# Performance work log

Hardware: AMD Instinct MI355X
Metric: run time of the kernel (lower is better)

Reference implementation:

```python
import jax, jax.numpy as jnp
import numpy as np

N_NODES = 100000
N_EDGES = 1600000
IN_DIM = 128
HEADS = 4
HEAD_DIM = 16  # hidden_dim 64 // 4 heads
HID = HEADS * HEAD_DIM
NEG_SLOPE = 0.2


def setup_inputs() -> dict:
    key = jax.random.key(0)
    ks = jax.random.split(key, 20)
    inp = {
        "x": jax.random.normal(ks[0], (N_NODES, IN_DIM), dtype=jnp.float32),
        "edge_index": jax.random.randint(ks[1], (2, N_EDGES), 0, N_NODES, dtype=jnp.int32),
    }
    dims = [IN_DIM, HID, HID]
    for l in range(3):
        d_in = dims[l]
        sc = 1.0 / np.sqrt(d_in)
        inp[f"w{l}"] = jax.random.normal(ks[2 + 4 * l], (d_in, HID), dtype=jnp.float32) * sc
        inp[f"asrc{l}"] = jax.random.normal(ks[3 + 4 * l], (HEADS, HEAD_DIM), dtype=jnp.float32) * 0.1
        inp[f"adst{l}"] = jax.random.normal(ks[4 + 4 * l], (HEADS, HEAD_DIM), dtype=jnp.float32) * 0.1
        inp[f"b{l}"] = jnp.zeros((HID,), dtype=jnp.float32)
    inp["out_w"] = jax.random.normal(ks[14], (HID, 1), dtype=jnp.float32) * (1.0 / np.sqrt(HID))
    inp["out_b"] = jnp.zeros((1,), dtype=jnp.float32)
    return inp


def _gat_layer(h, src, dst, W, a_src, a_dst, b):
    # h: [N, d_in]; src/dst: [E'] (self-loops already appended)
    n = h.shape[0]
    xh = (h @ W).reshape(n, HEADS, HEAD_DIM)              # [N,H,C]
    al_s = jnp.sum(xh * a_src, axis=-1)                   # [N,H]
    al_d = jnp.sum(xh * a_dst, axis=-1)                   # [N,H]
    e = jax.nn.leaky_relu(al_s[src] + al_d[dst], NEG_SLOPE)  # [E',H]
    # segment-softmax over incoming edges of each destination node
    m = jax.ops.segment_max(e, dst, num_segments=n)       # [N,H]
    p = jnp.exp(e - m[dst])
    z = jax.ops.segment_sum(p, dst, num_segments=n)       # [N,H]
    alpha = p / (z[dst] + 1e-16)                          # [E',H]
    msg = xh[src] * alpha[:, :, None]                     # [E',H,C]
    out = jax.ops.segment_sum(msg, dst, num_segments=n)   # [N,H,C]
    return out.reshape(n, HID) + b


def reference(x, edge_index, w0, asrc0, adst0, b0, w1, asrc1, adst1, b1,
              w2, asrc2, adst2, b2, out_w, out_b):
    n = x.shape[0]
    loops = jnp.arange(n, dtype=edge_index.dtype)
    src = jnp.concatenate([edge_index[0], loops])  # PyG GATConv adds self-loops
    dst = jnp.concatenate([edge_index[1], loops])
    h = x
    params = [(w0, asrc0, adst0, b0), (w1, asrc1, adst1, b1), (w2, asrc2, adst2, b2)]
    for W, a_s, a_d, b in params:
        h = _gat_layer(h, src, dst, W, a_s, a_d, b)
        h = jax.nn.relu(h)
    return (h @ out_w + out_b).squeeze(-1)  # [N]
```

## Files before the change

### kernel.cpp

```cpp
#include <hip/hip_runtime.h>


#define NBMAX 512
#define SCHUNK 4096
#define BCAP 8192
#define PADSLACK 768

typedef __attribute__((ext_vector_type(8))) short bf16x8;
typedef __attribute__((ext_vector_type(4))) float f32x4;

__device__ inline unsigned short bf16_rtn(float x) {
    union { float f; unsigned u; } a; a.f = x;
    return (unsigned short)((a.u + 0x7FFFu + ((a.u >> 16) & 1u)) >> 16);
}
__device__ inline float bf16_to_f(unsigned short s) {
    union { unsigned u; float f; } b; b.u = ((unsigned)s) << 16;
    return b.f;
}

__global__ __launch_bounds__(256) void k_init(int* __restrict__ bhist, int nb,
                                              float* __restrict__ als, float* __restrict__ xh, int n) {
    int i = blockIdx.x * 256 + threadIdx.x;
    if (i < nb) bhist[i] = 0;
    int j = i - NBMAX;
    if (j >= 0 && j < 4) als[(size_t)n * 4 + j] = -1e30f;
    int k = i - NBMAX - 4;
    if (k >= 0 && k < 64) xh[(size_t)n * 64 + k] = 0.f;
}

__global__ __launch_bounds__(256) void k_bhist(const int* __restrict__ dst, int* __restrict__ bhist, int e) {
    __shared__ unsigned int h[NBMAX];
    int t = threadIdx.x;
    h[t] = 0;
    h[t + 256] = 0;
    __syncthreads();
    for (int i = blockIdx.x * 256 + t; i < e; i += gridDim.x * 256)
        atomicAdd(&h[dst[i] >> 8], 1u);
    __syncthreads();
    if (h[t]) atomicAdd(&bhist[t], (int)h[t]);
    if (h[t + 256]) atomicAdd(&bhist[t + 256], (int)h[t + 256]);
}

__global__ __launch_bounds__(512) void k_bscan(const int* __restrict__ bhist, int* __restrict__ boffs,
                                               int* __restrict__ bfill, int nb, int e) {
    __shared__ int s[NBMAX];
    int t = threadIdx.x;
    int v = (t < nb) ? bhist[t] : 0;
    s[t] = v;
    __syncthreads();
    for (int o = 1; o < 512; o <<= 1) {
        int add = (t >= o) ? s[t - o] : 0;
        __syncthreads();
        s[t] += add;
        __syncthreads();
    }
    boffs[t] = s[t] - v;
    if (t == 511) boffs[512] = s[511];
    bfill[t] = 0;
}

__global__ __launch_bounds__(512) void k_bscatter(const int* __restrict__ src, const int* __restrict__ dst,
                                                  const int* __restrict__ boffs, int* __restrict__ bfill,
                                                  unsigned int* __restrict__ edata, int e) {
    __shared__ unsigned int hist[NBMAX];
    __shared__ unsigned int loc[NBMAX];
    __shared__ int gbase[NBMAX];
    __shared__ unsigned int stmp[NBMAX];
    __shared__ unsigned int sortbuf[SCHUNK];
    __shared__ int posbuf[SCHUNK];
    int t = threadIdx.x;
    int i0 = blockIdx.x * SCHUNK;
    int cnt = min(SCHUNK, e - i0);
    hist[t] = 0;
    __syncthreads();
    for (int j = t; j < cnt; j += 512) atomicAdd(&hist[dst[i0 + j] >> 8], 1u);
    __syncthreads();
    unsigned int v = hist[t];
    stmp[t] = v;
    __syncthreads();
    for (int o = 1; o < 512; o <<= 1) {
        unsigned int add = (t >= o) ? stmp[t - o] : 0;
        __syncthreads();
        stmp[t] += add;
        __syncthreads();
    }
    loc[t] = stmp[t] - v;
    int gb = 0;
    if (v > 0) gb = atomicAdd(&bfill[t], (int)v);
    gbase[t] = boffs[t] + gb - (int)loc[t];
    hist[t] = loc[t];
    __syncthreads();
    for (int j = t; j < cnt; j += 512) {
        int d = dst[i0 + j];
        int s = src[i0 + j];
        int b = d >> 8;
        unsigned int p = atomicAdd(&hist[b], 1u);
        sortbuf[p] = (unsigned int)s | ((unsigned int)(d & 255) << 24);
        posbuf[p] = gbase[b] + (int)p;
    }
    __syncthreads();
    for (int j = t; j < cnt; j += 512) edata[posbuf[j]] = sortbuf[j];
}

__global__ __launch_bounds__(256) void k_bfinal(const unsigned int* __restrict__ edata,
                                                const int* __restrict__ boffs, int* __restrict__ poffs,
                                                int* __restrict__ pend, int* __restrict__ ssrc,
                                                int n, int nb) {
    __shared__ unsigned int hist[256];
    __shared__ unsigned int stmp[256];
    __shared__ unsigned int loc[256];
    __shared__ unsigned int cnt_s[256];
    __shared__ unsigned int srcbuf[BCAP];
    int b = blockIdx.x;
    int t = threadIdx.x;
    int e0 = boffs[b], e1 = boffs[b + 1];
    int cnt = e1 - e0;
    int pb = e0 + b * PADSLACK;
    hist[t] = 0;
    __syncthreads();
    for (int j = t; j < cnt; j += 256) atomicAdd(&hist[edata[e0 + j] >> 24], 1u);
    __syncthreads();
    unsigned int v = hist[t];
    unsigned int v4 = (v + 3u) & ~3u;
    cnt_s[t] = v;
    stmp[t] = v4;
    __syncthreads();
    for (int o = 1; o < 256; o <<= 1) {
        unsigned int add = (t >= o) ? stmp[t - o] : 0;
        __syncthreads();
        stmp[t] += add;
        __syncthreads();
    }
    loc[t] = stmp[t] - v4;
    int ptot = (int)stmp[255];
    int node = b * 256 + t;
    if (node < n) {
        poffs[node] = pb + (int)loc[t];
        pend[node] = pb + (int)(loc[t] + v4);
    }
    hist[t] = loc[t];
    __syncthreads();
    if (cnt + PADSLACK <= BCAP) {
        for (int j = t; j < cnt; j += 256) {
            unsigned int p = edata[e0 + j];
            unsigned int pos = atomicAdd(&hist[p >> 24], 1u);
            srcbuf[pos] = p & 0xFFFFFFu;
        }
        for (unsigned int k = v; k < v4; ++k) srcbuf[loc[t] + k] = (unsigned int)n;
        __syncthreads();
        for (int j = t; j < ptot; j += 256) ssrc[pb + j] = (int)srcbuf[j];
    } else {
        for (int j = t; j < cnt; j += 256) {
            unsigned int p = edata[e0 + j];
            unsigned int pos = atomicAdd(&hist[p >> 24], 1u);
            ssrc[pb + (int)pos] = (int)(p & 0xFFFFFFu);
        }
        for (unsigned int k = v; k < v4; ++k) ssrc[pb + (int)(loc[t] + k)] = n;
    }
}

__global__ __launch_bounds__(256) void k_wprep(const float* __restrict__ w0, const float* __restrict__ w1,
                                               const float* __restrict__ w2,
                                               unsigned short* __restrict__ p0h, unsigned short* __restrict__ p0l,
                                               unsigned short* __restrict__ p1h, unsigned short* __restrict__ p1l,
                                               unsigned short* __restrict__ p2h, unsigned short* __restrict__ p2l) {
    int g = blockIdx.x * 256 + threadIdx.x;
    const float* W;
    unsigned short *ph, *pl;
    int idx;
    if (g < 1024) { W = w0; ph = p0h; pl = p0l; idx = g; }
    else if (g < 1536) { W = w1; ph = p1h; pl = p1l; idx = g - 1024; }
    else if (g < 2048) { W = w2; ph = p2h; pl = p2l; idx = g - 1536; }
    else return;
    int ko = idx >> 6, nn = idx & 63;
#pragma unroll
    for (int j = 0; j < 8; ++j) {
        float w = W[(size_t)(ko * 8 + j) * 64 + nn];
        unsigned short hb = bf16_rtn(w);
        ph[(size_t)idx * 8 + j] = hb;
        pl[(size_t)idx * 8 + j] = bf16_rtn(w - bf16_to_f(hb));
    }
}

template <int D_IN>
__global__ __launch_bounds__(256) void k_mgemm(const float* __restrict__ h,
                                               const unsigned short* __restrict__ wph,
                                               const unsigned short* __restrict__ wpl,
                                               const float* __restrict__ asrc, const float* __restrict__ adst,
                                               float* __restrict__ xh, float* __restrict__ als,
                                               float* __restrict__ ald, int n) {
    int t = threadIdx.x;
    int wv = t >> 6, lane = t & 63;
    int quad = lane >> 4, l16 = lane & 15;
    int m0 = blockIdx.x * 64 + wv * 16;
    int node_a = m0 + l16;
    int mm = min(node_a, n - 1);
    const float* hrow = h + (size_t)mm * D_IN + quad * 8;

    f32x4 acc[4];
#pragma unroll
    for (int i = 0; i < 4; ++i) acc[i] = (f32x4){0.f, 0.f, 0.f, 0.f};

    constexpr int KSTEPS = D_IN / 32;
#pragma unroll
    for (int s = 0; s < KSTEPS; ++s) {
        float4 a0 = *(const float4*)(hrow + s * 32);
        float4 a1 = *(const float4*)(hrow + s * 32 + 4);
        float av[8] = {a0.x, a0.y, a0.z, a0.w, a1.x, a1.y, a1.z, a1.w};
        bf16x8 ahi, alo;
#pragma unroll
        for (int j = 0; j < 8; ++j) {
            unsigned short hb = bf16_rtn(av[j]);
            ahi[j] = (short)hb;
            alo[j] = (short)bf16_rtn(av[j] - bf16_to_f(hb));
        }
        const unsigned short* bbase = wph + ((size_t)((s * 4 + quad) * 64 + l16)) * 8;
        const unsigned short* bbasel = wpl + ((size_t)((s * 4 + quad) * 64 + l16)) * 8;
#pragma unroll
        for (int nt = 0; nt < 4; ++nt) {
            bf16x8 bhi = *(const bf16x8*)(bbase + (size_t)nt * 16 * 8);
            bf16x8 blo = *(const bf16x8*)(bbasel + (size_t)nt * 16 * 8);
            acc[nt] = __builtin_amdgcn_mfma_f32_16x16x32_bf16(ahi, bhi, acc[nt], 0, 0, 0);
            acc[nt] = __builtin_amdgcn_mfma_f32_16x16x32_bf16(ahi, blo, acc[nt], 0, 0, 0);
            acc[nt] = __builtin_amdgcn_mfma_f32_16x16x32_bf16(alo, bhi, acc[nt], 0, 0, 0);
        }
    }
#pragma unroll
    for (int nt = 0; nt < 4; ++nt) {
        float as_l = asrc[nt * 16 + l16];
        float ad_l = adst[nt * 16 + l16];
#pragma unroll
        for (int r = 0; r < 4; ++r) {
            int node = m0 + quad * 4 + r;
            float c = acc[nt][r];
            if (node < n) xh[(size_t)node * 64 + nt * 16 + l16] = c;
            float ps = c * as_l, pd = c * ad_l;
            ps += __shfl_xor(ps, 1, 64); pd += __shfl_xor(pd, 1, 64);
            ps += __shfl_xor(ps, 2, 64); pd += __shfl_xor(pd, 2, 64);
            ps += __shfl_xor(ps, 4, 64); pd += __shfl_xor(pd, 4, 64);
            ps += __shfl_xor(ps, 8, 64); pd += __shfl_xor(pd, 8, 64);
            if (l16 == 0 && node < n) {
                als[node * 4 + nt] = ps;
                ald[node * 4 + nt] = pd;
            }
        }
    }
}

__device__ inline float4 lrelu4(float4 v) {
    float4 r;
    r.x = v.x >= 0.f ? v.x : 0.2f * v.x;
    r.y = v.y >= 0.f ? v.y : 0.2f * v.y;
    r.z = v.z >= 0.f ? v.z : 0.2f * v.z;
    r.w = v.w >= 0.f ? v.w : 0.2f * v.w;
    return r;
}

#define ACCUM(LO, HI, ACC, ZS)                                                  \
    {                                                                           \
        int g_ = ((LO) - s0) >> 2, gb_ = ((HI) - s0) >> 2;                      \
        for (; g_ + 4 <= gb_; g_ += 4) {                                        \
            int4 uu0 = *(const int4*)&ub[g_ * 4];                               \
            int4 uu1 = *(const int4*)&ub[g_ * 4 + 4];                           \
            int4 uu2 = *(const int4*)&ub[g_ * 4 + 8];                           \
            int4 uu3 = *(const int4*)&ub[g_ * 4 + 12];                          \
            float4 pp0 = *(const float4*)&per[g_ * 4];                          \
            float4 pp1 = *(const float4*)&per[g_ * 4 + 4];                      \
            float4 pp2 = *(const float4*)&per[g_ * 4 + 8];                      \
            float4 pp3 = *(const float4*)&per[g_ * 4 + 12];                     \
            float x0 = *(const float*)(xl + (size_t)(unsigned)uu0.x);           \
            float x1 = *(const float*)(xl + (size_t)(unsigned)uu0.y);           \
            float x2 = *(const float*)(xl + (size_t)(unsigned)uu0.z);           \
            float x3 = *(const float*)(xl + (size_t)(unsigned)uu0.w);           \
            float x4 = *(const float*)(xl + (size_t)(unsigned)uu1.x);           \
            float x5 = *(const float*)(xl + (size_t)(unsigned)uu1.y);           \
            float x6 = *(const float*)(xl + (size_t)(unsigned)uu1.z);           \
            float x7 = *(const float*)(xl + (size_t)(unsigned)uu1.w);           \
            float x8 = *(const float*)(xl + (size_t)(unsigned)uu2.x);           \
            float x9 = *(const float*)(xl + (size_t)(unsigned)uu2.y);           \
            float xa = *(const float*)(xl + (size_t)(unsigned)uu2.z);           \
            float xb = *(const float*)(xl + (size_t)(unsigned)uu2.w);           \
            float xc = *(const float*)(xl + (size_t)(unsigned)uu3.x);           \
            float xd = *(const float*)(xl + (size_t)(unsigned)uu3.y);           \
            float xe = *(const float*)(xl + (size_t)(unsigned)uu3.z);           \
            float xf = *(const float*)(xl + (size_t)(unsigned)uu3.w);           \
            ZS += pp0.x + pp0.y + pp0.z + pp0.w;                                \
            ZS += pp1.x + pp1.y + pp1.z + pp1.w;                                \
            ZS += pp2.x + pp2.y + pp2.z + pp2.w;                                \
            ZS += pp3.x + pp3.y + pp3.z + pp3.w;                                \
            ACC += pp0.x * x0; ACC += pp0.y * x1; ACC += pp0.z * x2; ACC += pp0.w * x3; \
            ACC += pp1.x * x4; ACC += pp1.y * x5; ACC += pp1.z * x6; ACC += pp1.w * x7; \
            ACC += pp2.x * x8; ACC += pp2.y * x9; ACC += pp2.z * xa; ACC += pp2.w * xb; \
            ACC += pp3.x * xc; ACC += pp3.y * xd; ACC += pp3.z * xe; ACC += pp3.w * xf; \
        }                                                                       \
        for (; g_ < gb_; ++g_) {                                                \
            int4 uu = *(const int4*)&ub[g_ * 4];                                \
            float4 pp = *(const float4*)&per[g_ * 4];                           \
            float x0 = *(const float*)(xl + (size_t)(unsigned)uu.x);            \
            float x1 = *(const float*)(xl + (size_t)(unsigned)uu.y);            \
            float x2 = *(const float*)(xl + (size_t)(unsigned)uu.z);            \
            float x3 = *(const float*)(xl + (size_t)(unsigned)uu.w);            \
            ZS += pp.x + pp.y + pp.z + pp.w;                                    \
            ACC += pp.x * x0; ACC += pp.y * x1; ACC += pp.z * x2; ACC += pp.w * x3; \
        }                                                                       \
    }

__global__ __launch_bounds__(256) void k_agg(const float* __restrict__ xh,
                                             const float* __restrict__ als, const float* __restrict__ ald,
                                             const int* __restrict__ poffs, const int* __restrict__ pend,
                                             const int* __restrict__ ssrc,
                                             const float* __restrict__ bias, float* __restrict__ hout,
                                             const float* __restrict__ outw, const float* __restrict__ outb,
                                             float* __restrict__ fout, int n) {
    __shared__ int s_u[4][64];
    __shared__ float s_pe[4][4][64];
    int wslot = threadIdx.x >> 6;
    int lane = threadIdx.x & 63;
    int w = (blockIdx.x * 256 + threadIdx.x) >> 6;
    int v0 = w << 2;
    if (v0 >= n) return;
    int head = lane >> 4;
    int* ub = s_u[wslot];
    float* per = s_pe[wslot][head];
    float* pew = &s_pe[wslot][0][lane];

    int vlast = n - 1;
    int last = min(v0 + 3, vlast);
    int4 rr = *(const int4*)(poffs + v0);
    int e3 = pend[last];
    int r0 = rr.x;
    int r1 = (v0 + 1 <= last) ? rr.y : e3;
    int r2 = (v0 + 2 <= last) ? rr.z : e3;
    int r3 = (v0 + 3 <= last) ? rr.w : e3;

    const char* xl = (const char*)(xh + lane);
    float acc0 = *(const float*)(xl + ((size_t)(unsigned)v0 << 8));
    float acc1 = *(const float*)(xl + ((size_t)(unsigned)min(v0 + 1, vlast) << 8));
    float acc2 = *(const float*)(xl + ((size_t)(unsigned)min(v0 + 2, vlast) << 8));
    float acc3 = *(const float*)(xl + ((size_t)(unsigned)min(v0 + 3, vlast) << 8));
    float zs0 = 0.f, zs1 = 0.f, zs2 = 0.f, zs3 = 0.f;

    for (int s0 = r0; s0 < e3; s0 += 64) {
        int cnt = min(64, e3 - s0);
        int e = s0 + lane;
        int u = n;
        if (lane < cnt) u = ssrc[e];
        int nid = v0 + (e >= r1) + (e >= r2) + (e >= r3);
        nid = min(nid, vlast);
        float4 alsd = *(const float4*)(als + 4 * (size_t)nid);
        float4 aldd = *(const float4*)(ald + 4 * (size_t)nid);
        float4 m4 = lrelu4(make_float4(alsd.x + aldd.x, alsd.y + aldd.y,
                                       alsd.z + aldd.z, alsd.w + aldd.w));
        float4 alu = *(const float4*)(als + 4 * (size_t)u);
        float4 e4 = lrelu4(make_float4(alu.x + aldd.x, alu.y + aldd.y,
                                       alu.z + aldd.z, alu.w + aldd.w));
        float4 pe;
        pe.x = __expf(e4.x - m4.x);
        pe.y = __expf(e4.y - m4.y);
        pe.z = __expf(e4.z - m4.z);
        pe.w = __expf(e4.w - m4.w);
        ub[lane] = u << 8;
        pew[0] = pe.x;
        pew[64] = pe.y;
        pew[128] = pe.z;
        pew[192] = pe.w;
        int lim = s0 + cnt;
        int hi0 = min(r1, lim);
        int lo1 = max(r1, s0), hi1 = min(r2, lim);
        int lo2 = max(r2, s0), hi2 = min(r3, lim);
        int lo3 = max(r3, s0);
        ACCUM(s0, hi0, acc0, zs0);
        ACCUM(lo1, hi1, acc1, zs1);
        ACCUM(lo2, hi2, acc2, zs2);
        ACCUM(lo3, lim, acc3, zs3);
    }

    float bl = bias[lane];
    float z0 = 1.f + zs0, z1 = 1.f + zs1, z2 = 1.f + zs2, z3 = 1.f + zs3;
    float o0 = fmaxf(acc0 / (z0 + 1e-16f) + bl, 0.f);
    float o1 = fmaxf(acc1 / (z1 + 1e-16f) + bl, 0.f);
    float o2 = fmaxf(acc2 / (z2 + 1e-16f) + bl, 0.f);
    float o3 = fmaxf(acc3 / (z3 + 1e-16f) + bl, 0.f);
    if (outw) {
        float ow = outw[lane];
        float ob = outb[0];
        float t0 = o0 * ow, t1 = o1 * ow, t2 = o2 * ow, t3 = o3 * ow;
#pragma unroll
        for (int d = 32; d; d >>= 1) {
            t0 += __shfl_down(t0, d, 64);
            t1 += __shfl_down(t1, d, 64);
            t2 += __shfl_down(t2, d, 64);
            t3 += __shfl_down(t3, d, 64);
        }
        if (lane == 0) {
            fout[v0] = t0 + ob;
            if (v0 + 1 < n) fout[v0 + 1] = t1 + ob;
            if (v0 + 2 < n) fout[v0 + 2] = t2 + ob;
            if (v0 + 3 < n) fout[v0 + 3] = t3 + ob;
        }
    } else {
        hout[((size_t)v0 << 6) + lane] = o0;
        if (v0 + 1 < n) hout[((size_t)(v0 + 1) << 6) + lane] = o1;
        if (v0 + 2 < n) hout[((size_t)(v0 + 2) << 6) + lane] = o2;
        if (v0 + 3 < n) hout[((size_t)(v0 + 3) << 6) + lane] = o3;
    }
}

extern "C" void kernel_launch(void* const* d_in, const int* in_sizes, int n_in,
                              void* d_out, int out_size, void* d_ws, size_t ws_size,
                              hipStream_t stream) {
    const float* x = (const float*)d_in[0];
    const int* ei = (const int*)d_in[1];
    const float* w[3] = {(const float*)d_in[2], (const float*)d_in[6], (const float*)d_in[10]};
    const float* as[3] = {(const float*)d_in[3], (const float*)d_in[7], (const float*)d_in[11]};
    const float* ad[3] = {(const float*)d_in[4], (const float*)d_in[8], (const float*)d_in[12]};
    const float* b[3] = {(const float*)d_in[5], (const float*)d_in[9], (const float*)d_in[13]};
    const float* outw = (const float*)d_in[14];
    const float* outb = (const float*)d_in[15];

    const int N = in_sizes[0] / 128;
    const int E = in_sizes[1] / 2;
    const int* src = ei;
    const int* dst = ei + E;
    const int NB = (N + 255) / 256;

    char* ws = (char*)d_ws;
    auto alloc = [&](size_t bytes) -> void* {
        void* p = (void*)ws;
        ws += (bytes + 255) & ~(size_t)255;
        return p;
    };
    int* bhist = (int*)alloc(NBMAX * 4);
    int* boffs = (int*)alloc((NBMAX + 1) * 4);
    int* bfill = (int*)alloc(NBMAX * 4);
    int* poffs = (int*)alloc((size_t)(N + 8) * 4);
    int* pend = (int*)alloc((size_t)N * 4);
    int* ssrc = (int*)alloc((size_t)(E + NBMAX * PADSLACK + 256) * 4);
    float* xh = (float*)alloc((size_t)(N + 1) * 64 * 4);
    float* hbuf = (float*)alloc((size_t)N * 64 * 4);
    float* als = (float*)alloc((size_t)(N + 1) * 4 * 4);
    float* ald = (float*)alloc((size_t)N * 4 * 4);
    unsigned short* p0h = (unsigned short*)alloc(8192 * 2);
    unsigned short* p0l = (unsigned short*)alloc(8192 * 2);
    unsigned short* p1h = (unsigned short*)alloc(4096 * 2);
    unsigned short* p1l = (unsigned short*)alloc(4096 * 2);
    unsigned short* p2h = (unsigned short*)alloc(4096 * 2);
    unsigned short* p2l = (unsigned short*)alloc(4096 * 2);
    unsigned int* edata = (unsigned int*)xh;

    k_wprep<<<8, 256, 0, stream>>>(w[0], w[1], w[2], p0h, p0l, p1h, p1l, p2h, p2l);
    k_init<<<3, 256, 0, stream>>>(bhist, NBMAX, als, xh, N);
    k_bhist<<<256, 256, 0, stream>>>(dst, bhist, E);
    k_bscan<<<1, 512, 0, stream>>>(bhist, boffs, bfill, NB, E);
    k_bscatter<<<(E + SCHUNK - 1) / SCHUNK, 512, 0, stream>>>(src, dst, boffs, bfill, edata, E);
    k_bfinal<<<NB, 256, 0, stream>>>(edata, boffs, poffs, pend, ssrc, N, NB);

    const int gblocks = (N + 63) / 64;
    const int ablocks = (N + 15) / 16;

    k_mgemm<128><<<gblocks, 256, 0, stream>>>(x, p0h, p0l, as[0], ad[0], xh, als, ald, N);
    k_agg<<<ablocks, 256, 0, stream>>>(xh, als, ald, poffs, pend, ssrc, b[0], hbuf, nullptr, nullptr, nullptr, N);
    k_mgemm<64><<<gblocks, 256, 0, stream>>>(hbuf, p1h, p1l, as[1], ad[1], xh, als, ald, N);
    k_agg<<<ablocks, 256, 0, stream>>>(xh, als, ald, poffs, pend, ssrc, b[1], hbuf, nullptr, nullptr, nullptr, N);
    k_mgemm<64><<<gblocks, 256, 0, stream>>>(hbuf, p2h, p2l, as[2], ad[2], xh, als, ald, N);
    k_agg<<<ablocks, 256, 0, stream>>>(xh, als, ald, poffs, pend, ssrc, b[2], nullptr, outw, outb, (float*)d_out, N);
}
```

Before: 434.3 us.

## Replace bucketed CSR build with degree-count scan scatter; prefetch and split accumulators in agg

```diff
diff --git a/kernel.cpp b/kernel.cpp
--- a/kernel.cpp
+++ b/kernel.cpp
@@ -1,10 +1,7 @@
 #include <hip/hip_runtime.h>
 
 
-#define NBMAX 512
-#define SCHUNK 4096
-#define BCAP 8192
-#define PADSLACK 768
+#define SCB 2048
 
 typedef __attribute__((ext_vector_type(8))) short bf16x8;
 typedef __attribute__((ext_vector_type(4))) float f32x4;
@@ -18,145 +15,97 @@
     return b.f;
 }
 
-__global__ __launch_bounds__(256) void k_init(int* __restrict__ bhist, int nb,
+__global__ __launch_bounds__(256) void k_init(int* __restrict__ deg,
                                               float* __restrict__ als, float* __restrict__ xh, int n) {
     int i = blockIdx.x * 256 + threadIdx.x;
-    if (i < nb) bhist[i] = 0;
-    int j = i - NBMAX;
-    if (j >= 0 && j < 4) als[(size_t)n * 4 + j] = -1e30f;
-    int k = i - NBMAX - 4;
-    if (k >= 0 && k < 64) xh[(size_t)n * 64 + k] = 0.f;
-}
-
-__global__ __launch_bounds__(256) void k_bhist(const int* __restrict__ dst, int* __restrict__ bhist, int e) {
-    __shared__ unsigned int h[NBMAX];
-    int t = threadIdx.x;
-    h[t] = 0;
-    h[t + 256] = 0;
-    __syncthreads();
-    for (int i = blockIdx.x * 256 + t; i < e; i += gridDim.x * 256)
-        atomicAdd(&h[dst[i] >> 8], 1u);
-    __syncthreads();
-    if (h[t]) atomicAdd(&bhist[t], (int)h[t]);
-    if (h[t + 256]) atomicAdd(&bhist[t + 256], (int)h[t + 256]);
-}
-
-__global__ __launch_bounds__(512) void k_bscan(const int* __restrict__ bhist, int* __restrict__ boffs,
-                                               int* __restrict__ bfill, int nb, int e) {
-    __shared__ int s[NBMAX];
-    int t = threadIdx.x;
-    int v = (t < nb) ? bhist[t] : 0;
-    s[t] = v;
-    __syncthreads();
-    for (int o = 1; o < 512; o <<= 1) {
-        int add = (t >= o) ? s[t - o] : 0;
-        __syncthreads();
-        s[t] += add;
-        __syncthreads();
-    }
-    boffs[t] = s[t] - v;
-    if (t == 511) boffs[512] = s[511];
-    bfill[t] = 0;
-}
-
-__global__ __launch_bounds__(512) void k_bscatter(const int* __restrict__ src, const int* __restrict__ dst,
-                                                  const int* __restrict__ boffs, int* __restrict__ bfill,
-                                                  unsigned int* __restrict__ edata, int e) {
-    __shared__ unsigned int hist[NBMAX];
-    __shared__ unsigned int loc[NBMAX];
-    __shared__ int gbase[NBMAX];
-    __shared__ unsigned int stmp[NBMAX];
-    __shared__ unsigned int sortbuf[SCHUNK];
-    __shared__ int posbuf[SCHUNK];
-    int t = threadIdx.x;
-    int i0 = blockIdx.x * SCHUNK;
-    int cnt = min(SCHUNK, e - i0);
-    hist[t] = 0;
-    __syncthreads();
-    for (int j = t; j < cnt; j += 512) atomicAdd(&hist[dst[i0 + j] >> 8], 1u);
-    __syncthreads();
-    unsigned int v = hist[t];
-    stmp[t] = v;
-    __syncthreads();
-    for (int o = 1; o < 512; o <<= 1) {
-        unsigned int add = (t >= o) ? stmp[t - o] : 0;
-        __syncthreads();
-        stmp[t] += add;
-        __syncthreads();
-    }
-    loc[t] = stmp[t] - v;
-    int gb = 0;
-    if (v > 0) gb = atomicAdd(&bfill[t], (int)v);
-    gbase[t] = boffs[t] + gb - (int)loc[t];
-    hist[t] = loc[t];
-    __syncthreads();
-    for (int j = t; j < cnt; j += 512) {
-        int d = dst[i0 + j];
-        int s = src[i0 + j];
-        int b = d >> 8;
-        unsigned int p = atomicAdd(&hist[b], 1u);
-        sortbuf[p] = (unsigned int)s | ((unsigned int)(d & 255) << 24);
-        posbuf[p] = gbase[b] + (int)p;
-    }
-    __syncthreads();
-    for (int j = t; j < cnt; j += 512) edata[posbuf[j]] = sortbuf[j];
-}
-
-__global__ __launch_bounds__(256) void k_bfinal(const unsigned int* __restrict__ edata,
-                                                const int* __restrict__ boffs, int* __restrict__ poffs,
-                                                int* __restrict__ pend, int* __restrict__ ssrc,
-                                                int n, int nb) {
-    __shared__ unsigned int hist[256];
-    __shared__ unsigned int stmp[256];
-    __shared__ unsigned int loc[256];
-    __shared__ unsigned int cnt_s[256];
-    __shared__ unsigned int srcbuf[BCAP];
-    int b = blockIdx.x;
-    int t = threadIdx.x;
-    int e0 = boffs[b], e1 = boffs[b + 1];
-    int cnt = e1 - e0;
-    int pb = e0 + b * PADSLACK;
-    hist[t] = 0;
-    __syncthreads();
-    for (int j = t; j < cnt; j += 256) atomicAdd(&hist[edata[e0 + j] >> 24], 1u);
-    __syncthreads();
-    unsigned int v = hist[t];
-    unsigned int v4 = (v + 3u) & ~3u;
-    cnt_s[t] = v;
-    stmp[t] = v4;
+    if (i < n) deg[i] = 0;
+    if (i < 4) als[(size_t)n * 4 + i] = -1e30f;
+    if (i < 64) xh[(size_t)n * 64 + i] = 0.f;
+}
+
+__global__ __launch_bounds__(256) void k_deg(const int* __restrict__ dst, int* __restrict__ deg, int e) {
+    int i = blockIdx.x * 256 + threadIdx.x;
+    if (i < e) atomicAdd(&deg[dst[i]], 1);
+}
+
+__global__ __launch_bounds__(256) void k_scan1(const int* __restrict__ deg, int* __restrict__ loc,
+                                               int* __restrict__ bsum, int n) {
+    __shared__ int ts[256];
+    int b = blockIdx.x, t = threadIdx.x;
+    int base = b * SCB + t * 8;
+    int d[8], s = 0;
+    if (base + 8 <= n) {
+        int4 a = *(const int4*)(deg + base);
+        int4 c = *(const int4*)(deg + base + 4);
+        int dv[8] = {a.x, a.y, a.z, a.w, c.x, c.y, c.z, c.w};
+#pragma unroll
+        for (int k = 0; k < 8; ++k) { d[k] = s; s += (dv[k] + 3) & ~3; }
+    } else {
+#pragma unroll
+        for (int k = 0; k < 8; ++k) {
+            d[k] = s;
+            int v = (base + k < n) ? deg[base + k] : 0;
+            s += (v + 3) & ~3;
+        }
+    }
+    ts[t] = s;
     __syncthreads();
     for (int o = 1; o < 256; o <<= 1) {
-        unsigned int add = (t >= o) ? stmp[t - o] : 0;
+        int add = (t >= o) ? ts[t - o] : 0;
         __syncthreads();
-        stmp[t] += add;
+        ts[t] += add;
         __syncthreads();
     }
-    loc[t] = stmp[t] - v4;
-    int ptot = (int)stmp[255];
-    int node = b * 256 + t;
-    if (node < n) {
-        poffs[node] = pb + (int)loc[t];
-        pend[node] = pb + (int)(loc[t] + v4);
-    }
-    hist[t] = loc[t];
-    __syncthreads();
-    if (cnt + PADSLACK <= BCAP) {
-        for (int j = t; j < cnt; j += 256) {
-            unsigned int p = edata[e0 + j];
-            unsigned int pos = atomicAdd(&hist[p >> 24], 1u);
-            srcbuf[pos] = p & 0xFFFFFFu;
-        }
-        for (unsigned int k = v; k < v4; ++k) srcbuf[loc[t] + k] = (unsigned int)n;
-        __syncthreads();
-        for (int j = t; j < ptot; j += 256) ssrc[pb + j] = (int)srcbuf[j];
+    int excl = ts[t] - s;
+    if (base + 8 <= n) {
+        int4 o0 = {excl + d[0], excl + d[1], excl + d[2], excl + d[3]};
+        int4 o1 = {excl + d[4], excl + d[5], excl + d[6], excl + d[7]};
+        *(int4*)(loc + base) = o0;
+        *(int4*)(loc + base + 4) = o1;
     } else {
-        for (int j = t; j < cnt; j += 256) {
-            unsigned int p = edata[e0 + j];
-            unsigned int pos = atomicAdd(&hist[p >> 24], 1u);
-            ssrc[pb + (int)pos] = (int)(p & 0xFFFFFFu);
-        }
-        for (unsigned int k = v; k < v4; ++k) ssrc[pb + (int)(loc[t] + k)] = n;
-    }
+        for (int k = 0; k < 8; ++k)
+            if (base + k < n) loc[base + k] = excl + d[k];
+    }
+    if (t == 255) bsum[b] = ts[255];
+}
+
+__global__ __launch_bounds__(64) void k_scan2(int* __restrict__ bsum, int nb) {
+    int t = threadIdx.x;
+    int v = (t < nb) ? bsum[t] : 0;
+#pragma unroll
+    for (int o = 1; o < 64; o <<= 1) {
+        int u = __shfl_up(v, o, 64);
+        if (t >= o) v += u;
+    }
+    if (t < nb) bsum[t] = v;
+}
+
+__global__ __launch_bounds__(256) void k_scan3(const int* __restrict__ deg, const int* __restrict__ loc,
+                                               const int* __restrict__ bsum, int* __restrict__ poffs,
+                                               int* __restrict__ pend, int* __restrict__ cursor, int n) {
+    int i = blockIdx.x * 256 + threadIdx.x;
+    if (i >= n) return;
+    int b = i >> 11;
+    int base = b ? bsum[b - 1] : 0;
+    int p = base + loc[i];
+    int d4 = (deg[i] + 3) & ~3;
+    poffs[i] = p;
+    pend[i] = p + d4;
+    cursor[i] = p;
+}
+
+__global__ __launch_bounds__(256) void k_fill(int4* __restrict__ ssrc4, int n, int tot4) {
+    int i = blockIdx.x * 256 + threadIdx.x;
+    if (i < tot4) ssrc4[i] = (int4){n, n, n, n};
+}
+
+__global__ __launch_bounds__(256) void k_scatter(const int* __restrict__ src, const int* __restrict__ dst,
+                                                 int* __restrict__ cursor, int* __restrict__ ssrc, int e) {
+    int i = blockIdx.x * 256 + threadIdx.x;
+    if (i >= e) return;
+    int d = dst[i];
+    int p = atomicAdd(&cursor[d], 1);
+    ssrc[p] = src[i];
 }
 
 __global__ __launch_bounds__(256) void k_wprep(const float* __restrict__ w0, const float* __restrict__ w1,
@@ -188,7 +137,7 @@
                                                const unsigned short* __restrict__ wpl,
                                                const float* __restrict__ asrc, const float* __restrict__ adst,
                                                float* __restrict__ xh, float* __restrict__ als,
-                                               float* __restrict__ ald, int n) {
+                                               float* __restrict__ ald, float* __restrict__ mvec, int n) {
     int t = threadIdx.x;
     int wv = t >> 6, lane = t & 63;
     int quad = lane >> 4, l16 = lane & 15;
@@ -242,6 +191,8 @@
             if (l16 == 0 && node < n) {
                 als[node * 4 + nt] = ps;
                 ald[node * 4 + nt] = pd;
+                float sm = ps + pd;
+                mvec[node * 4 + nt] = sm >= 0.f ? sm : 0.2f * sm;
             }
         }
     }
@@ -256,7 +207,7 @@
     return r;
 }
 
-#define ACCUM(LO, HI, ACC, ZS)                                                  \
+#define ACCUM(LO, HI, ACCA, ACCB, ZS)                                           \
     {                                                                           \
         int g_ = ((LO) - s0) >> 2, gb_ = ((HI) - s0) >> 2;                      \
         for (; g_ + 4 <= gb_; g_ += 4) {                                        \
@@ -288,10 +239,14 @@
             ZS += pp1.x + pp1.y + pp1.z + pp1.w;                                \
             ZS += pp2.x + pp2.y + pp2.z + pp2.w;                                \
             ZS += pp3.x + pp3.y + pp3.z + pp3.w;                                \
-            ACC += pp0.x * x0; ACC += pp0.y * x1; ACC += pp0.z * x2; ACC += pp0.w * x3; \
-            ACC += pp1.x * x4; ACC += pp1.y * x5; ACC += pp1.z * x6; ACC += pp1.w * x7; \
-            ACC += pp2.x * x8; ACC += pp2.y * x9; ACC += pp2.z * xa; ACC += pp2.w * xb; \
-            ACC += pp3.x * xc; ACC += pp3.y * xd; ACC += pp3.z * xe; ACC += pp3.w * xf; \
+            ACCA += pp0.x * x0; ACCB += pp0.y * x1;                             \
+            ACCA += pp0.z * x2; ACCB += pp0.w * x3;                             \
+            ACCA += pp1.x * x4; ACCB += pp1.y * x5;                             \
+            ACCA += pp1.z * x6; ACCB += pp1.w * x7;                             \
+            ACCA += pp2.x * x8; ACCB += pp2.y * x9;                             \
+            ACCA += pp2.z * xa; ACCB += pp2.w * xb;                             \
+            ACCA += pp3.x * xc; ACCB += pp3.y * xd;                             \
+            ACCA += pp3.z * xe; ACCB += pp3.w * xf;                             \
         }                                                                       \
         for (; g_ < gb_; ++g_) {                                                \
             int4 uu = *(const int4*)&ub[g_ * 4];                                \
@@ -301,12 +256,14 @@
             float x2 = *(const float*)(xl + (size_t)(unsigned)uu.z);            \
             float x3 = *(const float*)(xl + (size_t)(unsigned)uu.w);            \
             ZS += pp.x + pp.y + pp.z + pp.w;                                    \
-            ACC += pp.x * x0; ACC += pp.y * x1; ACC += pp.z * x2; ACC += pp.w * x3; \
+            ACCA += pp.x * x0; ACCB += pp.y * x1;                               \
+            ACCA += pp.z * x2; ACCB += pp.w * x3;                               \
         }                                                                       \
     }
 
 __global__ __launch_bounds__(256) void k_agg(const float* __restrict__ xh,
                                              const float* __restrict__ als, const float* __restrict__ ald,
+                                             const float* __restrict__ mvec,
                                              const int* __restrict__ poffs, const int* __restrict__ pend,
                                              const int* __restrict__ ssrc,
                                              const float* __restrict__ bias, float* __restrict__ hout,
@@ -334,53 +291,65 @@
     int r3 = (v0 + 3 <= last) ? rr.w : e3;
 
     const char* xl = (const char*)(xh + lane);
-    float acc0 = *(const float*)(xl + ((size_t)(unsigned)v0 << 8));
-    float acc1 = *(const float*)(xl + ((size_t)(unsigned)min(v0 + 1, vlast) << 8));
-    float acc2 = *(const float*)(xl + ((size_t)(unsigned)min(v0 + 2, vlast) << 8));
-    float acc3 = *(const float*)(xl + ((size_t)(unsigned)min(v0 + 3, vlast) << 8));
+    float acc0a = *(const float*)(xl + ((size_t)(unsigned)v0 << 8));
+    float acc1a = *(const float*)(xl + ((size_t)(unsigned)min(v0 + 1, vlast) << 8));
+    float acc2a = *(const float*)(xl + ((size_t)(unsigned)min(v0 + 2, vlast) << 8));
+    float acc3a = *(const float*)(xl + ((size_t)(unsigned)min(v0 + 3, vlast) << 8));
+    float acc0b = 0.f, acc1b = 0.f, acc2b = 0.f, acc3b = 0.f;
     float zs0 = 0.f, zs1 = 0.f, zs2 = 0.f, zs3 = 0.f;
 
-    for (int s0 = r0; s0 < e3; s0 += 64) {
+    int s0 = r0;
+    int u_n = n;
+    if (s0 < e3) {
+        if (lane < e3 - s0) u_n = ssrc[s0 + lane];
+    }
+    float4 alu_n = *(const float4*)(als + 4 * (size_t)u_n);
+    int e_n = s0 + lane;
+    int nid_n = min(v0 + (e_n >= r1) + (e_n >= r2) + (e_n >= r3), vlast);
+    float4 ald_n = *(const float4*)(ald + 4 * (size_t)nid_n);
+    float4 m_n = *(const float4*)(mvec + 4 * (size_t)nid_n);
+
+    while (s0 < e3) {
         int cnt = min(64, e3 - s0);
-        int e = s0 + lane;
-        int u = n;
-        if (lane < cnt) u = ssrc[e];
-        int nid = v0 + (e >= r1) + (e >= r2) + (e >= r3);
-        nid = min(nid, vlast);
-        float4 alsd = *(const float4*)(als + 4 * (size_t)nid);
-        float4 aldd = *(const float4*)(ald + 4 * (size_t)nid);
-        float4 m4 = lrelu4(make_float4(alsd.x + aldd.x, alsd.y + aldd.y,
-                                       alsd.z + aldd.z, alsd.w + aldd.w));
-        float4 alu = *(const float4*)(als + 4 * (size_t)u);
-        float4 e4 = lrelu4(make_float4(alu.x + aldd.x, alu.y + aldd.y,
-                                       alu.z + aldd.z, alu.w + aldd.w));
+        float4 e4 = lrelu4(make_float4(alu_n.x + ald_n.x, alu_n.y + ald_n.y,
+                                       alu_n.z + ald_n.z, alu_n.w + ald_n.w));
         float4 pe;
-        pe.x = __expf(e4.x - m4.x);
-        pe.y = __expf(e4.y - m4.y);
-        pe.z = __expf(e4.z - m4.z);
-        pe.w = __expf(e4.w - m4.w);
-        ub[lane] = u << 8;
+        pe.x = __expf(e4.x - m_n.x);
+        pe.y = __expf(e4.y - m_n.y);
+        pe.z = __expf(e4.z - m_n.z);
+        pe.w = __expf(e4.w - m_n.w);
+        ub[lane] = u_n << 8;
         pew[0] = pe.x;
         pew[64] = pe.y;
         pew[128] = pe.z;
         pew[192] = pe.w;
+        int s1 = s0 + 64;
+        if (s1 < e3) {
+            u_n = n;
+            if (lane < e3 - s1) u_n = ssrc[s1 + lane];
+            alu_n = *(const float4*)(als + 4 * (size_t)u_n);
+            int e1 = s1 + lane;
+            int nid1 = min(v0 + (e1 >= r1) + (e1 >= r2) + (e1 >= r3), vlast);
+            ald_n = *(const float4*)(ald + 4 * (size_t)nid1);
+            m_n = *(const float4*)(mvec + 4 * (size_t)nid1);
+        }
         int lim = s0 + cnt;
         int hi0 = min(r1, lim);
         int lo1 = max(r1, s0), hi1 = min(r2, lim);
         int lo2 = max(r2, s0), hi2 = min(r3, lim);
         int lo3 = max(r3, s0);
-        ACCUM(s0, hi0, acc0, zs0);
-        ACCUM(lo1, hi1, acc1, zs1);
-        ACCUM(lo2, hi2, acc2, zs2);
-        ACCUM(lo3, lim, acc3, zs3);
+        ACCUM(s0, hi0, acc0a, acc0b, zs0);
+        ACCUM(lo1, hi1, acc1a, acc1b, zs1);
+        ACCUM(lo2, hi2, acc2a, acc2b, zs2);
+        ACCUM(lo3, lim, acc3a, acc3b, zs3);
+        s0 = s1;
     }
 
     float bl = bias[lane];
-    float z0 = 1.f + zs0, z1 = 1.f + zs1, z2 = 1.f + zs2, z3 = 1.f + zs3;
-    float o0 = fmaxf(acc0 / (z0 + 1e-16f) + bl, 0.f);
-    float o1 = fmaxf(acc1 / (z1 + 1e-16f) + bl, 0.f);
-    float o2 = fmaxf(acc2 / (z2 + 1e-16f) + bl, 0.f);
-    float o3 = fmaxf(acc3 / (z3 + 1e-16f) + bl, 0.f);
+    float o0 = fmaxf((acc0a + acc0b) / (1.f + zs0 + 1e-16f) + bl, 0.f);
+    float o1 = fmaxf((acc1a + acc1b) / (1.f + zs1 + 1e-16f) + bl, 0.f);
+    float o2 = fmaxf((acc2a + acc2b) / (1.f + zs2 + 1e-16f) + bl, 0.f);
+    float o3 = fmaxf((acc3a + acc3b) / (1.f + zs3 + 1e-16f) + bl, 0.f);
     if (outw) {
         float ow = outw[lane];
         float ob = outb[0];
@@ -422,7 +391,8 @@
     const int E = in_sizes[1] / 2;
     const int* src = ei;
     const int* dst = ei + E;
-    const int NB = (N + 255) / 256;
+    const int NS1 = (N + SCB - 1) / SCB;
+    const int SS = E + 3 * N + 256;
 
     char* ws = (char*)d_ws;
     auto alloc = [&](size_t bytes) -> void* {
@@ -430,38 +400,44 @@
         ws += (bytes + 255) & ~(size_t)255;
         return p;
     };
-    int* bhist = (int*)alloc(NBMAX * 4);
-    int* boffs = (int*)alloc((NBMAX + 1) * 4);
-    int* bfill = (int*)alloc(NBMAX * 4);
+    int* deg = (int*)alloc((size_t)N * 4);
+    int* loc = (int*)alloc((size_t)N * 4);
+    int* bsum = (int*)alloc(64 * 4);
     int* poffs = (int*)alloc((size_t)(N + 8) * 4);
     int* pend = (int*)alloc((size_t)N * 4);
-    int* ssrc = (int*)alloc((size_t)(E + NBMAX * PADSLACK + 256) * 4);
+    int* cursor = (int*)alloc((size_t)N * 4);
+    int* ssrc = (int*)alloc((size_t)SS * 4);
     float* xh = (float*)alloc((size_t)(N + 1) * 64 * 4);
     float* hbuf = (float*)alloc((size_t)N * 64 * 4);
     float* als = (float*)alloc((size_t)(N + 1) * 4 * 4);
     float* ald = (float*)alloc((size_t)N * 4 * 4);
+    float* mvec = (float*)alloc((size_t)N * 4 * 4);
     unsigned short* p0h = (unsigned short*)alloc(8192 * 2);
     unsigned short* p0l = (unsigned short*)alloc(8192 * 2);
     unsigned short* p1h = (unsigned short*)alloc(4096 * 2);
     unsigned short* p1l = (unsigned short*)alloc(4096 * 2);
     unsigned short* p2h = (unsigned short*)alloc(4096 * 2);
     unsigned short* p2l = (unsigned short*)alloc(4096 * 2);
-    unsigned int* edata = (unsigned int*)xh;
+
+    const int nblk = (N + 255) / 256;
+    const int eblk = (E + 255) / 256;
 
     k_wprep<<<8, 256, 0, stream>>>(w[0], w[1], w[2], p0h, p0l, p1h, p1l, p2h, p2l);
-    k_init<<<3, 256, 0, stream>>>(bhist, NBMAX, als, xh, N);
-    k_bhist<<<256, 256, 0, stream>>>(dst, bhist, E);
-    k_bscan<<<1, 512, 0, stream>>>(bhist, boffs, bfill, NB, E);
-    k_bscatter<<<(E + SCHUNK - 1) / SCHUNK, 512, 0, stream>>>(src, dst, boffs, bfill, edata, E);
-    k_bfinal<<<NB, 256, 0, stream>>>(edata, boffs, poffs, pend, ssrc, N, NB);
+    k_init<<<nblk, 256, 0, stream>>>(deg, als, xh, N);
+    k_deg<<<eblk, 256, 0, stream>>>(dst, deg, E);
+    k_scan1<<<NS1, 256, 0, stream>>>(deg, loc, bsum, N);
+    k_scan2<<<1, 64, 0, stream>>>(bsum, NS1);
+    k_scan3<<<nblk, 256, 0, stream>>>(deg, loc, bsum, poffs, pend, cursor, N);
+    k_fill<<<(SS / 4 + 255) / 256, 256, 0, stream>>>((int4*)ssrc, N, SS / 4);
+    k_scatter<<<eblk, 256, 0, stream>>>(src, dst, cursor, ssrc, E);
 
     const int gblocks = (N + 63) / 64;
     const int ablocks = (N + 15) / 16;
 
-    k_mgemm<128><<<gblocks, 256, 0, stream>>>(x, p0h, p0l, as[0], ad[0], xh, als, ald, N);
-    k_agg<<<ablocks, 256, 0, stream>>>(xh, als, ald, poffs, pend, ssrc, b[0], hbuf, nullptr, nullptr, nullptr, N);
-    k_mgemm<64><<<gblocks, 256, 0, stream>>>(hbuf, p1h, p1l, as[1], ad[1], xh, als, ald, N);
-    k_agg<<<ablocks, 256, 0, stream>>>(xh, als, ald, poffs, pend, ssrc, b[1], hbuf, nullptr, nullptr, nullptr, N);
-    k_mgemm<64><<<gblocks, 256, 0, stream>>>(hbuf, p2h, p2l, as[2], ad[2], xh, als, ald, N);
-    k_agg<<<ablocks, 256, 0, stream>>>(xh, als, ald, poffs, pend, ssrc, b[2], nullptr, outw, outb, (float*)d_out, N);
-}
+    k_mgemm<128><<<gblocks, 256, 0, stream>>>(x, p0h, p0l, as[0], ad[0], xh, als, ald, mvec, N);
+    k_agg<<<ablocks, 256, 0, stream>>>(xh, als, ald, mvec, poffs, pend, ssrc, b[0], hbuf, nullptr, nullptr, nullptr, N);
+    k_mgemm<64><<<gblocks, 256, 0, stream>>>(hbuf, p1h, p1l, as[1], ad[1], xh, als, ald, mvec, N);
+    k_agg<<<ablocks, 256, 0, stream>>>(xh, als, ald, mvec, poffs, pend, ssrc, b[1], hbuf, nullptr, nullptr, nullptr, N);
+    k_mgemm<64><<<gblocks, 256, 0, stream>>>(hbuf, p2h, p2l, as[2], ad[2], xh, als, ald, mvec, N);
+    k_agg<<<ablocks, 256, 0, stream>>>(xh, als, ald, mvec, poffs, pend, ssrc, b[2], nullptr, outw, outb, (float*)d_out, N);
+}
```

Result: slower. 583.5 us (+34.4%).
